# Performance work log

Hardware: AMD Instinct MI355X
Metric: run time of the kernel (lower is better)

## Reference

```python
import jax, jax.numpy as jnp
import numpy as np

B, F, D = 16384, 256, 128
H = [512, 256]
OUT = 8
VOCAB = 100000


def setup_inputs() -> dict:
    key = jax.random.key(0)
    ks = jax.random.split(key, 16)
    s = lambda k, *sh: jax.random.normal(k, sh, jnp.float32) * 0.05
    return dict(
        features=jax.random.normal(ks[0], (B, F), jnp.float32),
        ent_idx=jax.random.randint(ks[1], (B,), 0, VOCAB),
        target=jax.random.randint(ks[2], (B,), 0, OUT),
        Wf=s(ks[3], F, D), bf=jnp.zeros((D,), jnp.float32),
        Wu=s(ks[4], D, D), bu=jnp.zeros((D,), jnp.float32),
        w_cf=s(ks[5], D), w_fc=s(ks[6], D),
        w_ef=s(ks[7], D), w_fe=s(ks[8], D),
        b_c=jnp.zeros((1,), jnp.float32), b_e=jnp.zeros((1,), jnp.float32),
        head_tab=s(ks[9], VOCAB, D), ent_tab=s(ks[10], VOCAB, D),
        W0=s(ks[11], 2 * D, H[0]), b0=jnp.zeros((H[0],), jnp.float32),
        W1=s(ks[12], H[0], H[1]), b1=jnp.zeros((H[1],), jnp.float32),
        W2=s(ks[13], H[1], OUT), b2=jnp.zeros((OUT,), jnp.float32),
    )


def cross_compress(f, e, w_cf, w_fc, w_ef, w_fe, b_c, b_e):
    # torch code builds c = f (outer) e of shape (B,D,D) then matmuls a (D,1)
    # vector; algebraically (f e^T) w = f * (e . w), so we use the O(B*D) form.
    ew_cf = e @ w_cf  # (B,)
    fw_fc = f @ w_fc
    ew_ef = e @ w_ef
    fw_fe = f @ w_fe
    new_f = f * ew_cf[:, None] + e * fw_fc[:, None] + b_c
    new_e = f * ew_ef[:, None] + e * fw_fe[:, None] + b_e
    return new_f, new_e


def reference(features, ent_idx, target, Wf, bf, Wu, bu, w_cf, w_fc, w_ef,
              w_fe, b_c, b_e, head_tab, ent_tab, W0, b0, W1, b1, W2, b2):
    # 'rec' branch of CompanyOperationEvaluation.forward (eval mode, dropout=id)
    cf = jax.nn.relu(features @ Wf + bf)          # feature_layer
    e = ent_tab[ent_idx]                           # entity_embed lookup
    h = head_tab[ent_idx]                          # head_embed lookup (same ids)
    for _ in range(2):
        cf = jax.nn.relu(cf @ Wu + bu)             # user_low_mlp_layer
        h, e = cross_compress(h, e, w_cf, w_fc, w_ef, w_fe, b_c, b_e)
    high = jnp.concatenate([cf, e], axis=1)        # (B, 2D)
    x = jax.nn.relu(high @ W0 + b0)
    x = jax.nn.relu(x @ W1 + b1)
    x = jax.nn.relu(x @ W2 + b2)                   # pred_last_layer
    prob = jax.nn.softmax(x, axis=1)
    return (prob, target)
```

## Files before the change

kernel.cpp:

```cpp
#include <hip/hip_runtime.h>
#include <hip/hip_bf16.h>


typedef __bf16 bf16x8 __attribute__((ext_vector_type(8)));
typedef float floatx4 __attribute__((ext_vector_type(4)));

__device__ __forceinline__ unsigned short f2bf(float x) {
  unsigned int u = __builtin_bit_cast(unsigned int, x);
  u = (u + 0x7FFFu + ((u >> 16) & 1u)) >> 16;
  return (unsigned short)u;
}

#define PHASE_BAR()                                      \
  do {                                                   \
    asm volatile("s_waitcnt lgkmcnt(0)" ::: "memory");   \
    __builtin_amdgcn_s_barrier();                        \
    __builtin_amdgcn_sched_barrier(0);                   \
  } while (0)

__global__ __launch_bounds__(256) void prep_kernel(
    const int* __restrict__ ent_idx, const float* __restrict__ head_tab,
    const float* __restrict__ ent_tab,
    const float* __restrict__ w_cf, const float* __restrict__ w_fc,
    const float* __restrict__ w_ef, const float* __restrict__ w_fe,
    const float* __restrict__ b_c, const float* __restrict__ b_e,
    const float* __restrict__ Wf, const float* __restrict__ Wu,
    const float* __restrict__ W0, const float* __restrict__ W1,
    const float* __restrict__ W2,
    unsigned short* __restrict__ high,
    unsigned short* __restrict__ wfT, unsigned short* __restrict__ wuT,
    unsigned short* __restrict__ w0T, unsigned short* __restrict__ w1T,
    unsigned short* __restrict__ w2T) {
  __shared__ unsigned short tile[32][34];
  const int bid = blockIdx.x, tid = threadIdx.x;
  if (bid < 2048) {
    const int row = bid * 8 + (tid >> 5);
    const int c = (tid & 31) * 4;
    const int idx = ent_idx[row];
    float4 hv = *(const float4*)(head_tab + (size_t)idx * 128 + c);
    float4 ev = *(const float4*)(ent_tab + (size_t)idx * 128 + c);
    float h[4] = {hv.x, hv.y, hv.z, hv.w};
    float e[4] = {ev.x, ev.y, ev.z, ev.w};
    float wcf[4], wfc[4], wef[4], wfe[4];
#pragma unroll
    for (int j = 0; j < 4; ++j) {
      wcf[j] = w_cf[c + j]; wfc[j] = w_fc[c + j];
      wef[j] = w_ef[c + j]; wfe[j] = w_fe[c + j];
    }
    const float bc = b_c[0], be = b_e[0];
#pragma unroll
    for (int it = 0; it < 2; ++it) {
      float d0 = 0, d1 = 0, d2 = 0, d3 = 0;
#pragma unroll
      for (int j = 0; j < 4; ++j) {
        d0 += e[j] * wcf[j]; d1 += h[j] * wfc[j];
        d2 += e[j] * wef[j]; d3 += h[j] * wfe[j];
      }
#pragma unroll
      for (int s = 1; s < 32; s <<= 1) {
        d0 += __shfl_xor(d0, s); d1 += __shfl_xor(d1, s);
        d2 += __shfl_xor(d2, s); d3 += __shfl_xor(d3, s);
      }
      float nh[4], ne[4];
#pragma unroll
      for (int j = 0; j < 4; ++j) {
        nh[j] = h[j] * d0 + e[j] * d1 + bc;
        ne[j] = h[j] * d2 + e[j] * d3 + be;
      }
#pragma unroll
      for (int j = 0; j < 4; ++j) { h[j] = nh[j]; e[j] = ne[j]; }
    }
    uint2 v;
    v.x = (unsigned)f2bf(e[0]) | ((unsigned)f2bf(e[1]) << 16);
    v.y = (unsigned)f2bf(e[2]) | ((unsigned)f2bf(e[3]) << 16);
    *(uint2*)(high + (size_t)row * 256 + 128 + c) = v;
  } else if (bid < 2352) {
    int t = bid - 2048;
    const float* src; unsigned short* dst; int N, K, kt, nt;
    if (t < 32)       { src = Wf; dst = wfT; N = 128; K = 256; kt = t >> 2;       nt = t & 3; }
    else if (t < 48)  { t -= 32;  src = Wu; dst = wuT; N = 128; K = 128; kt = t >> 2; nt = t & 3; }
    else if (t < 176) { t -= 48;  src = W0; dst = w0T; N = 512; K = 256; kt = t >> 4; nt = t & 15; }
    else              { t -= 176; src = W1; dst = w1T; N = 256; K = 512; kt = t >> 3; nt = t & 7; }
    {
      int r = tid >> 3, cg = (tid & 7) * 4;
      float4 v = *(const float4*)(src + (size_t)(kt * 32 + r) * N + nt * 32 + cg);
      tile[r][cg + 0] = f2bf(v.x); tile[r][cg + 1] = f2bf(v.y);
      tile[r][cg + 2] = f2bf(v.z); tile[r][cg + 3] = f2bf(v.w);
    }
    __syncthreads();
    {
      int rp = tid >> 3, cg = (tid & 7) * 4;
      uint2 o;
      o.x = (unsigned)tile[cg + 0][rp] | ((unsigned)tile[cg + 1][rp] << 16);
      o.y = (unsigned)tile[cg + 2][rp] | ((unsigned)tile[cg + 3][rp] << 16);
      *(uint2*)(dst + (size_t)(nt * 32 + rp) * K + kt * 32 + cg) = o;
    }
  } else {
#pragma unroll
    for (int i = 0; i < 8; ++i) {
      int g = tid * 8 + i, k = g >> 3, n = g & 7;
      w2T[n * 256 + k] = f2bf(W2[g]);
    }
  }
}

template <int LDK>
__device__ __forceinline__ void loadB(uint4 (&r)[4],
                                      const unsigned short* __restrict__ p,
                                      int tid) {
#pragma unroll
  for (int i = 0; i < 4; ++i) {
    int chunk = i * 256 + tid, row = chunk >> 3, seg = chunk & 7;
    r[i] = *(const uint4*)(p + (size_t)row * LDK + seg * 8);
  }
}

__device__ __forceinline__ void dsw(unsigned short* b, const uint4 (&r)[4],
                                    int tid) {
#pragma unroll
  for (int i = 0; i < 4; ++i) {
    int chunk = i * 256 + tid, row = chunk >> 3, seg = chunk & 7;
    *(uint4*)&b[row * 72 + seg * 8] = r[i];
  }
}

template <int PASS_STEPS, int LDK>
__device__ __forceinline__ const unsigned short* srcstep(
    const unsigned short* __restrict__ s, int st) {
  return s + (size_t)(st / PASS_STEPS) * 128 * LDK + (st % PASS_STEPS) * 64;
}

template <int LDA>
__device__ __forceinline__ void mstep(const unsigned short* A,
                                      const unsigned short* b, int k0,
                                      floatx4* acc, int m16, int quad,
                                      int wave) {
#pragma unroll
  for (int kk = 0; kk < 64; kk += 32) {
    bf16x8 a0 = *(const bf16x8*)&A[m16 * LDA + k0 + kk + quad * 8];
    bf16x8 a1 = *(const bf16x8*)&A[(16 + m16) * LDA + k0 + kk + quad * 8];
    bf16x8 b0 = *(const bf16x8*)&b[(wave * 32 + m16) * 72 + kk + quad * 8];
    bf16x8 b1 = *(const bf16x8*)&b[(wave * 32 + 16 + m16) * 72 + kk + quad * 8];
    acc[0] = __builtin_amdgcn_mfma_f32_16x16x32_bf16(a0, b0, acc[0], 0, 0, 0);
    acc[1] = __builtin_amdgcn_mfma_f32_16x16x32_bf16(a0, b1, acc[1], 0, 0, 0);
    acc[2] = __builtin_amdgcn_mfma_f32_16x16x32_bf16(a1, b0, acc[2], 0, 0, 0);
    acc[3] = __builtin_amdgcn_mfma_f32_16x16x32_bf16(a1, b1, acc[3], 0, 0, 0);
  }
}

template <int T, int LDA, int PASS_STEPS, int LDK>
__device__ __forceinline__ void gemm_phase(
    const unsigned short* A, const unsigned short* __restrict__ src,
    unsigned short* b_sh, floatx4* acc, int tid, int m16, int quad, int wave) {
  uint4 r[2][4];
  loadB<LDK>(r[0], srcstep<PASS_STEPS, LDK>(src, 0), tid);
  dsw(b_sh, r[0], tid);
  loadB<LDK>(r[1], srcstep<PASS_STEPS, LDK>(src, 1), tid);
  PHASE_BAR();
#pragma unroll
  for (int t = 0; t < T; ++t) {
    unsigned short* bcur = b_sh + (t & 1) * 9216;
    unsigned short* bnxt = b_sh + ((t + 1) & 1) * 9216;
    if (t + 2 < T) loadB<LDK>(r[t & 1], srcstep<PASS_STEPS, LDK>(src, t + 2), tid);
    mstep<LDA>(A, bcur, (t % PASS_STEPS) * 64, acc + (t / PASS_STEPS) * 4, m16,
               quad, wave);
    if (t + 1 < T) dsw(bnxt, r[(t + 1) & 1], tid);
    PHASE_BAR();
  }
}

__global__ __launch_bounds__(256, 2) void fused_mlp_kernel(
    const float* __restrict__ features, const unsigned short* __restrict__ wfT,
    const unsigned short* __restrict__ wuT, const float* __restrict__ bf_,
    const float* __restrict__ bu, const unsigned short* __restrict__ high,
    const unsigned short* __restrict__ w0T, const float* __restrict__ b0,
    const unsigned short* __restrict__ w1T, const float* __restrict__ b1,
    const unsigned short* __restrict__ w2T, const float* __restrict__ b2,
    const int* __restrict__ target, float* __restrict__ out) {
  __shared__ __align__(16) unsigned short regionA[17152];
  __shared__ __align__(16) unsigned short b_sh[2 * 9216];
  __shared__ __align__(16) unsigned short w2_sh[2048];
  unsigned short* feat_sh = regionA;
  unsigned short* buf0 = regionA + 8448;
  unsigned short* buf1 = regionA + 12800;
  unsigned short* A_sh = regionA;
  unsigned short* x0_sh = regionA;
  unsigned short* x1_sh = b_sh;

  const int tid = threadIdx.x;
  const int r0 = blockIdx.x * 32;
  const int lane = tid & 63, wave = tid >> 6;
  const int m16 = lane & 15, quad = lane >> 4;

  const int hrow = tid >> 4, hseg = (tid & 15) * 8;
  uint4 hv0 = *(const uint4*)(high + (size_t)(r0 + hrow) * 256 + 128 + hseg);
  uint4 hv1 = *(const uint4*)(high + (size_t)(r0 + 16 + hrow) * 256 + 128 + hseg);
  *(uint4*)&w2_sh[tid * 8] = *(const uint4*)(w2T + tid * 8);

#pragma unroll
  for (int i = 0; i < 8; ++i) {
    int idx4 = i * 256 + tid;
    int row = idx4 >> 6, c = (idx4 & 63) * 4;
    float4 v = *(const float4*)(features + (size_t)(r0 + row) * 256 + c);
    uint2 o;
    o.x = (unsigned)f2bf(v.x) | ((unsigned)f2bf(v.y) << 16);
    o.y = (unsigned)f2bf(v.z) | ((unsigned)f2bf(v.w) << 16);
    *(uint2*)&feat_sh[row * 264 + c] = o;
  }

  floatx4 acc[4];
#pragma unroll
  for (int j = 0; j < 4; ++j) acc[j] = (floatx4){0.f, 0.f, 0.f, 0.f};
  gemm_phase<4, 264, 4, 256>(feat_sh, wfT, b_sh, acc, tid, m16, quad, wave);
#pragma unroll
  for (int mi = 0; mi < 2; ++mi)
#pragma unroll
    for (int ni = 0; ni < 2; ++ni) {
      int col = wave * 32 + ni * 16 + m16;
      float bv = bf_[col];
#pragma unroll
      for (int r = 0; r < 4; ++r)
        buf0[(mi * 16 + quad * 4 + r) * 136 + col] =
            f2bf(fmaxf(acc[mi * 2 + ni][r] + bv, 0.f));
    }
  *(uint4*)&A_sh[hrow * 264 + 128 + hseg] = hv0;
  *(uint4*)&A_sh[(16 + hrow) * 264 + 128 + hseg] = hv1;

#pragma unroll
  for (int j = 0; j < 4; ++j) acc[j] = (floatx4){0.f, 0.f, 0.f, 0.f};
  gemm_phase<2, 136, 2, 128>(buf0, wuT, b_sh, acc, tid, m16, quad, wave);
#pragma unroll
  for (int mi = 0; mi < 2; ++mi)
#pragma unroll
    for (int ni = 0; ni < 2; ++ni) {
      int col = wave * 32 + ni * 16 + m16;
      float bv = bu[col];
#pragma unroll
      for (int r = 0; r < 4; ++r)
        buf1[(mi * 16 + quad * 4 + r) * 136 + col] =
            f2bf(fmaxf(acc[mi * 2 + ni][r] + bv, 0.f));
    }

#pragma unroll
  for (int j = 0; j < 4; ++j) acc[j] = (floatx4){0.f, 0.f, 0.f, 0.f};
  gemm_phase<2, 136, 2, 128>(buf1, wuT, b_sh, acc, tid, m16, quad, wave);
#pragma unroll
  for (int mi = 0; mi < 2; ++mi)
#pragma unroll
    for (int ni = 0; ni < 2; ++ni) {
      int col = wave * 32 + ni * 16 + m16;
      float bv = bu[col];
#pragma unroll
      for (int r = 0; r < 4; ++r)
        A_sh[(mi * 16 + quad * 4 + r) * 264 + col] =
            f2bf(fmaxf(acc[mi * 2 + ni][r] + bv, 0.f));
    }

  floatx4 acc16[16];
#pragma unroll
  for (int j = 0; j < 16; ++j) acc16[j] = (floatx4){0.f, 0.f, 0.f, 0.f};
  gemm_phase<16, 264, 4, 256>(A_sh, w0T, b_sh, acc16, tid, m16, quad, wave);
#pragma unroll
  for (int np = 0; np < 4; ++np)
#pragma unroll
    for (int mi = 0; mi < 2; ++mi)
#pragma unroll
      for (int ni = 0; ni < 2; ++ni) {
        int col = np * 128 + wave * 32 + ni * 16 + m16;
        float bv = b0[col];
#pragma unroll
        for (int r = 0; r < 4; ++r)
          x0_sh[(mi * 16 + quad * 4 + r) * 520 + col] =
              f2bf(fmaxf(acc16[np * 4 + mi * 2 + ni][r] + bv, 0.f));
      }

  floatx4 acc8[8];
#pragma unroll
  for (int j = 0; j < 8; ++j) acc8[j] = (floatx4){0.f, 0.f, 0.f, 0.f};
  gemm_phase<16, 520, 8, 512>(x0_sh, w1T, b_sh, acc8, tid, m16, quad, wave);
#pragma unroll
  for (int np = 0; np < 2; ++np)
#pragma unroll
    for (int mi = 0; mi < 2; ++mi)
#pragma unroll
      for (int ni = 0; ni < 2; ++ni) {
        int col = np * 128 + wave * 32 + ni * 16 + m16;
        float bv = b1[col];
#pragma unroll
        for (int r = 0; r < 4; ++r)
          x1_sh[(mi * 16 + quad * 4 + r) * 264 + col] =
              f2bf(fmaxf(acc8[np * 4 + mi * 2 + ni][r] + bv, 0.f));
      }
  PHASE_BAR();

  {
    int row = tid >> 3, q = tid & 7;
    float p[8];
#pragma unroll
    for (int n = 0; n < 8; ++n) p[n] = 0.f;
#pragma unroll
    for (int jb = 0; jb < 4; ++jb) {
      bf16x8 xv = *(const bf16x8*)&x1_sh[row * 264 + q * 32 + jb * 8];
#pragma unroll
      for (int n = 0; n < 8; ++n) {
        bf16x8 wv = *(const bf16x8*)&w2_sh[n * 256 + q * 32 + jb * 8];
#pragma unroll
        for (int j = 0; j < 8; ++j) p[n] += (float)xv[j] * (float)wv[j];
      }
    }
#pragma unroll
    for (int s = 1; s < 8; s <<= 1)
#pragma unroll
      for (int n = 0; n < 8; ++n) p[n] += __shfl_xor(p[n], s);
    if (q == 0) {
      float mx = -1e30f;
#pragma unroll
      for (int n = 0; n < 8; ++n) {
        p[n] = fmaxf(p[n] + b2[n], 0.f);
        mx = fmaxf(mx, p[n]);
      }
      float sum = 0.f;
#pragma unroll
      for (int n = 0; n < 8; ++n) { p[n] = __expf(p[n] - mx); sum += p[n]; }
      const float inv = 1.f / sum;
      const int gr = r0 + row;
      float4 o0 = {p[0] * inv, p[1] * inv, p[2] * inv, p[3] * inv};
      float4 o1 = {p[4] * inv, p[5] * inv, p[6] * inv, p[7] * inv};
      *(float4*)(out + (size_t)gr * 8) = o0;
      *(float4*)(out + (size_t)gr * 8 + 4) = o1;
      out[16384 * 8 + gr] = (float)target[gr];
    }
  }
}

extern "C" void kernel_launch(void* const* d_in, const int* in_sizes, int n_in,
                              void* d_out, int out_size, void* d_ws, size_t ws_size,
                              hipStream_t stream) {
  const float* features = (const float*)d_in[0];
  const int* ent_idx    = (const int*)d_in[1];
  const int* target     = (const int*)d_in[2];
  const float* Wf  = (const float*)d_in[3];
  const float* bf_ = (const float*)d_in[4];
  const float* Wu  = (const float*)d_in[5];
  const float* bu  = (const float*)d_in[6];
  const float* w_cf = (const float*)d_in[7];
  const float* w_fc = (const float*)d_in[8];
  const float* w_ef = (const float*)d_in[9];
  const float* w_fe = (const float*)d_in[10];
  const float* b_c  = (const float*)d_in[11];
  const float* b_e  = (const float*)d_in[12];
  const float* head_tab = (const float*)d_in[13];
  const float* ent_tab  = (const float*)d_in[14];
  const float* W0 = (const float*)d_in[15];
  const float* b0 = (const float*)d_in[16];
  const float* W1 = (const float*)d_in[17];
  const float* b1 = (const float*)d_in[18];
  const float* W2 = (const float*)d_in[19];
  const float* b2 = (const float*)d_in[20];
  float* out = (float*)d_out;

  unsigned short* ws = (unsigned short*)d_ws;
  size_t off = 0;
  auto alloc = [&](size_t n) { unsigned short* p = ws + off; off += n; return p; };
  unsigned short* high = alloc(16384ull * 256);
  unsigned short* wfT  = alloc(32768);
  unsigned short* wuT  = alloc(16384);
  unsigned short* w0T  = alloc(131072);
  unsigned short* w1T  = alloc(131072);
  unsigned short* w2T  = alloc(2048);
  (void)ws_size; (void)in_sizes; (void)n_in; (void)out_size;

  prep_kernel<<<2353, 256, 0, stream>>>(ent_idx, head_tab, ent_tab,
      w_cf, w_fc, w_ef, w_fe, b_c, b_e, Wf, Wu, W0, W1, W2,
      high, wfT, wuT, w0T, w1T, w2T);
  fused_mlp_kernel<<<512, 256, 0, stream>>>(features, wfT, wuT, bf_, bu,
      high, w0T, b0, w1T, b1, w2T, b2, target, out);
}
```

Measured before the change: 188.2 us.

## Fuse embedding gather and cross-compress into MLP kernel; deepen weight prefetch

Moves the entity/head embedding gather and the two cross-compress iterations out of the prep kernel and into the fused MLP kernel. The gather is issued at kernel start and its loads overlap the first GEMM. This removes the bf16 'high' intermediate round trip through global memory and shrinks the prep grid. It also deepens the B-operand register prefetch from two to three steps, and reuses the Wu tiles already in shared memory for the second Wu GEMM instead of reloading them. The cost is more register pressure from 32 live floats per thread across the first GEMM and the triple prefetch buffer, which may hurt occupancy at launch bounds of 2 blocks.

```diff
diff --git a/kernel.cpp b/kernel.cpp
--- a/kernel.cpp
+++ b/kernel.cpp
@@ -19,63 +19,16 @@
   } while (0)
 
 __global__ __launch_bounds__(256) void prep_kernel(
-    const int* __restrict__ ent_idx, const float* __restrict__ head_tab,
-    const float* __restrict__ ent_tab,
-    const float* __restrict__ w_cf, const float* __restrict__ w_fc,
-    const float* __restrict__ w_ef, const float* __restrict__ w_fe,
-    const float* __restrict__ b_c, const float* __restrict__ b_e,
     const float* __restrict__ Wf, const float* __restrict__ Wu,
     const float* __restrict__ W0, const float* __restrict__ W1,
     const float* __restrict__ W2,
-    unsigned short* __restrict__ high,
     unsigned short* __restrict__ wfT, unsigned short* __restrict__ wuT,
     unsigned short* __restrict__ w0T, unsigned short* __restrict__ w1T,
     unsigned short* __restrict__ w2T) {
   __shared__ unsigned short tile[32][34];
   const int bid = blockIdx.x, tid = threadIdx.x;
-  if (bid < 2048) {
-    const int row = bid * 8 + (tid >> 5);
-    const int c = (tid & 31) * 4;
-    const int idx = ent_idx[row];
-    float4 hv = *(const float4*)(head_tab + (size_t)idx * 128 + c);
-    float4 ev = *(const float4*)(ent_tab + (size_t)idx * 128 + c);
-    float h[4] = {hv.x, hv.y, hv.z, hv.w};
-    float e[4] = {ev.x, ev.y, ev.z, ev.w};
-    float wcf[4], wfc[4], wef[4], wfe[4];
-#pragma unroll
-    for (int j = 0; j < 4; ++j) {
-      wcf[j] = w_cf[c + j]; wfc[j] = w_fc[c + j];
-      wef[j] = w_ef[c + j]; wfe[j] = w_fe[c + j];
-    }
-    const float bc = b_c[0], be = b_e[0];
-#pragma unroll
-    for (int it = 0; it < 2; ++it) {
-      float d0 = 0, d1 = 0, d2 = 0, d3 = 0;
-#pragma unroll
-      for (int j = 0; j < 4; ++j) {
-        d0 += e[j] * wcf[j]; d1 += h[j] * wfc[j];
-        d2 += e[j] * wef[j]; d3 += h[j] * wfe[j];
-      }
-#pragma unroll
-      for (int s = 1; s < 32; s <<= 1) {
-        d0 += __shfl_xor(d0, s); d1 += __shfl_xor(d1, s);
-        d2 += __shfl_xor(d2, s); d3 += __shfl_xor(d3, s);
-      }
-      float nh[4], ne[4];
-#pragma unroll
-      for (int j = 0; j < 4; ++j) {
-        nh[j] = h[j] * d0 + e[j] * d1 + bc;
-        ne[j] = h[j] * d2 + e[j] * d3 + be;
-      }
-#pragma unroll
-      for (int j = 0; j < 4; ++j) { h[j] = nh[j]; e[j] = ne[j]; }
-    }
-    uint2 v;
-    v.x = (unsigned)f2bf(e[0]) | ((unsigned)f2bf(e[1]) << 16);
-    v.y = (unsigned)f2bf(e[2]) | ((unsigned)f2bf(e[3]) << 16);
-    *(uint2*)(high + (size_t)row * 256 + 128 + c) = v;
-  } else if (bid < 2352) {
-    int t = bid - 2048;
+  if (bid < 304) {
+    int t = bid;
     const float* src; unsigned short* dst; int N, K, kt, nt;
     if (t < 32)       { src = Wf; dst = wfT; N = 128; K = 256; kt = t >> 2;       nt = t & 3; }
     else if (t < 48)  { t -= 32;  src = Wu; dst = wuT; N = 128; K = 128; kt = t >> 2; nt = t & 3; }
@@ -152,27 +105,32 @@
 __device__ __forceinline__ void gemm_phase(
     const unsigned short* A, const unsigned short* __restrict__ src,
     unsigned short* b_sh, floatx4* acc, int tid, int m16, int quad, int wave) {
-  uint4 r[2][4];
+  uint4 r[3][4];
   loadB<LDK>(r[0], srcstep<PASS_STEPS, LDK>(src, 0), tid);
   dsw(b_sh, r[0], tid);
-  loadB<LDK>(r[1], srcstep<PASS_STEPS, LDK>(src, 1), tid);
+  if (T > 1) loadB<LDK>(r[1], srcstep<PASS_STEPS, LDK>(src, 1), tid);
+  if (T > 2) loadB<LDK>(r[2], srcstep<PASS_STEPS, LDK>(src, 2), tid);
   PHASE_BAR();
 #pragma unroll
   for (int t = 0; t < T; ++t) {
-    unsigned short* bcur = b_sh + (t & 1) * 9216;
-    unsigned short* bnxt = b_sh + ((t + 1) & 1) * 9216;
-    if (t + 2 < T) loadB<LDK>(r[t & 1], srcstep<PASS_STEPS, LDK>(src, t + 2), tid);
-    mstep<LDA>(A, bcur, (t % PASS_STEPS) * 64, acc + (t / PASS_STEPS) * 4, m16,
-               quad, wave);
-    if (t + 1 < T) dsw(bnxt, r[(t + 1) & 1], tid);
+    if (t + 3 < T)
+      loadB<LDK>(r[t % 3], srcstep<PASS_STEPS, LDK>(src, t + 3), tid);
+    mstep<LDA>(A, b_sh + (t & 1) * 9216, (t % PASS_STEPS) * 64,
+               acc + (t / PASS_STEPS) * 4, m16, quad, wave);
+    if (t + 1 < T) dsw(b_sh + ((t + 1) & 1) * 9216, r[(t + 1) % 3], tid);
     PHASE_BAR();
   }
 }
 
 __global__ __launch_bounds__(256, 2) void fused_mlp_kernel(
-    const float* __restrict__ features, const unsigned short* __restrict__ wfT,
+    const float* __restrict__ features, const int* __restrict__ ent_idx,
+    const float* __restrict__ head_tab, const float* __restrict__ ent_tab,
+    const float* __restrict__ w_cf, const float* __restrict__ w_fc,
+    const float* __restrict__ w_ef, const float* __restrict__ w_fe,
+    const float* __restrict__ b_c, const float* __restrict__ b_e,
+    const unsigned short* __restrict__ wfT,
     const unsigned short* __restrict__ wuT, const float* __restrict__ bf_,
-    const float* __restrict__ bu, const unsigned short* __restrict__ high,
+    const float* __restrict__ bu,
     const unsigned short* __restrict__ w0T, const float* __restrict__ b0,
     const unsigned short* __restrict__ w1T, const float* __restrict__ b1,
     const unsigned short* __restrict__ w2T, const float* __restrict__ b2,
@@ -180,6 +138,7 @@
   __shared__ __align__(16) unsigned short regionA[17152];
   __shared__ __align__(16) unsigned short b_sh[2 * 9216];
   __shared__ __align__(16) unsigned short w2_sh[2048];
+  __shared__ __align__(16) float cw_sh[512];
   unsigned short* feat_sh = regionA;
   unsigned short* buf0 = regionA + 8448;
   unsigned short* buf1 = regionA + 12800;
@@ -192,9 +151,21 @@
   const int lane = tid & 63, wave = tid >> 6;
   const int m16 = lane & 15, quad = lane >> 4;
 
-  const int hrow = tid >> 4, hseg = (tid & 15) * 8;
-  uint4 hv0 = *(const uint4*)(high + (size_t)(r0 + hrow) * 256 + 128 + hseg);
-  uint4 hv1 = *(const uint4*)(high + (size_t)(r0 + 16 + hrow) * 256 + 128 + hseg);
+  const int grow = tid >> 3, gpart = tid & 7;
+  const int gidx = ent_idx[r0 + grow];
+  const float* hp = head_tab + (size_t)gidx * 128 + gpart * 16;
+  const float* ep = ent_tab + (size_t)gidx * 128 + gpart * 16;
+  float4 h4[4], e4[4];
+#pragma unroll
+  for (int j = 0; j < 4; ++j) {
+    h4[j] = *(const float4*)(hp + j * 4);
+    e4[j] = *(const float4*)(ep + j * 4);
+  }
+  if (tid < 128) {
+    int a = tid >> 5, o = (tid & 31) * 4;
+    const float* s = (a == 0) ? w_cf : (a == 1) ? w_fc : (a == 2) ? w_ef : w_fe;
+    *(float4*)&cw_sh[a * 128 + o] = *(const float4*)(s + o);
+  }
   *(uint4*)&w2_sh[tid * 8] = *(const uint4*)(w2T + tid * 8);
 
 #pragma unroll
@@ -223,8 +194,54 @@
         buf0[(mi * 16 + quad * 4 + r) * 136 + col] =
             f2bf(fmaxf(acc[mi * 2 + ni][r] + bv, 0.f));
     }
-  *(uint4*)&A_sh[hrow * 264 + 128 + hseg] = hv0;
-  *(uint4*)&A_sh[(16 + hrow) * 264 + 128 + hseg] = hv1;
+
+  {
+    float h[16], e[16];
+#pragma unroll
+    for (int j = 0; j < 4; ++j) {
+      h[4 * j + 0] = h4[j].x; h[4 * j + 1] = h4[j].y;
+      h[4 * j + 2] = h4[j].z; h[4 * j + 3] = h4[j].w;
+      e[4 * j + 0] = e4[j].x; e[4 * j + 1] = e4[j].y;
+      e[4 * j + 2] = e4[j].z; e[4 * j + 3] = e4[j].w;
+    }
+    const float bc = b_c[0], be = b_e[0];
+#pragma unroll
+    for (int it = 0; it < 2; ++it) {
+      float d0 = 0.f, d1 = 0.f, d2 = 0.f, d3 = 0.f;
+#pragma unroll
+      for (int j = 0; j < 16; ++j) {
+        float wcf = cw_sh[0 * 128 + gpart * 16 + j];
+        float wfc = cw_sh[1 * 128 + gpart * 16 + j];
+        float wef = cw_sh[2 * 128 + gpart * 16 + j];
+        float wfe = cw_sh[3 * 128 + gpart * 16 + j];
+        d0 += e[j] * wcf; d1 += h[j] * wfc;
+        d2 += e[j] * wef; d3 += h[j] * wfe;
+      }
+#pragma unroll
+      for (int s = 1; s < 8; s <<= 1) {
+        d0 += __shfl_xor(d0, s); d1 += __shfl_xor(d1, s);
+        d2 += __shfl_xor(d2, s); d3 += __shfl_xor(d3, s);
+      }
+#pragma unroll
+      for (int j = 0; j < 16; ++j) {
+        float nh = h[j] * d0 + e[j] * d1 + bc;
+        float ne = h[j] * d2 + e[j] * d3 + be;
+        h[j] = nh; e[j] = ne;
+      }
+    }
+    uint4 o0, o1;
+    unsigned* w = (unsigned*)&o0;
+#pragma unroll
+    for (int j = 0; j < 4; ++j)
+      w[j] = (unsigned)f2bf(e[2 * j]) | ((unsigned)f2bf(e[2 * j + 1]) << 16);
+    w = (unsigned*)&o1;
+#pragma unroll
+    for (int j = 0; j < 4; ++j)
+      w[j] = (unsigned)f2bf(e[8 + 2 * j]) |
+             ((unsigned)f2bf(e[8 + 2 * j + 1]) << 16);
+    *(uint4*)&A_sh[grow * 264 + 128 + gpart * 16] = o0;
+    *(uint4*)&A_sh[grow * 264 + 128 + gpart * 16 + 8] = o1;
+  }
 
 #pragma unroll
   for (int j = 0; j < 4; ++j) acc[j] = (floatx4){0.f, 0.f, 0.f, 0.f};
@@ -243,7 +260,10 @@
 
 #pragma unroll
   for (int j = 0; j < 4; ++j) acc[j] = (floatx4){0.f, 0.f, 0.f, 0.f};
-  gemm_phase<2, 136, 2, 128>(buf1, wuT, b_sh, acc, tid, m16, quad, wave);
+  PHASE_BAR();
+  mstep<136>(buf1, b_sh, 0, acc, m16, quad, wave);
+  mstep<136>(buf1, b_sh + 9216, 64, acc, m16, quad, wave);
+  PHASE_BAR();
 #pragma unroll
   for (int mi = 0; mi < 2; ++mi)
 #pragma unroll
@@ -362,7 +382,6 @@
   unsigned short* ws = (unsigned short*)d_ws;
   size_t off = 0;
   auto alloc = [&](size_t n) { unsigned short* p = ws + off; off += n; return p; };
-  unsigned short* high = alloc(16384ull * 256);
   unsigned short* wfT  = alloc(32768);
   unsigned short* wuT  = alloc(16384);
   unsigned short* w0T  = alloc(131072);
@@ -370,9 +389,9 @@
   unsigned short* w2T  = alloc(2048);
   (void)ws_size; (void)in_sizes; (void)n_in; (void)out_size;
 
-  prep_kernel<<<2353, 256, 0, stream>>>(ent_idx, head_tab, ent_tab,
-      w_cf, w_fc, w_ef, w_fe, b_c, b_e, Wf, Wu, W0, W1, W2,
-      high, wfT, wuT, w0T, w1T, w2T);
-  fused_mlp_kernel<<<512, 256, 0, stream>>>(features, wfT, wuT, bf_, bu,
-      high, w0T, b0, w1T, b1, w2T, b2, target, out);
-}
+  prep_kernel<<<305, 256, 0, stream>>>(Wf, Wu, W0, W1, W2,
+                                       wfT, wuT, w0T, w1T, w2T);
+  fused_mlp_kernel<<<512, 256, 0, stream>>>(features, ent_idx, head_tab,
+      ent_tab, w_cf, w_fc, w_ef, w_fe, b_c, b_e, wfT, wuT, bf_, bu,
+      w0T, b0, w1T, b1, w2T, b2, target, out);
+}
```

Measured after the change: 184.9 us. No clear change (-1.7%).
